# Kernel tuning notes

Measured on AMD Instinct MI355X. Metric: run time of the kernel, lower is better.

Reference implementation:

```python
import jax, jax.numpy as jnp
import numpy as np

N_NODES = 50000
N_EDGES = 800000
DIM_FEAT = 96
INFO_DIM = 32
DIM_EMB = 160
CONV_OUT = DIM_EMB - INFO_DIM  # 128
NUM_LAYERS = 3
NUM_GRAPHS = 500
DIM_TARGET = 10


def setup_inputs() -> dict:
    key = jax.random.key(0)
    ks = jax.random.split(key, 20)
    inp = {
        'x': jax.random.normal(ks[0], (N_NODES, DIM_FEAT), dtype=jnp.float32),
        'edge_index': jax.random.randint(ks[1], (2, N_EDGES), 0, N_NODES, dtype=jnp.int32),
        'batch': jnp.sort(jax.random.randint(ks[2], (N_NODES,), 0, NUM_GRAPHS, dtype=jnp.int32)),
        'struc_info': jax.random.normal(ks[3], (NUM_GRAPHS, INFO_DIM), dtype=jnp.float32),
    }
    # SAGEConv params per layer: lin_l (on aggregated neighbors, with bias), lin_r (on root, no bias)
    in_dims = [DIM_FEAT + INFO_DIM, DIM_EMB, DIM_EMB]
    k = 4
    for i, din in enumerate(in_dims):
        s = 1.0 / np.sqrt(din)
        inp[f'Wl{i}'] = jax.random.uniform(ks[k], (din, CONV_OUT), jnp.float32, -s, s); k += 1
        inp[f'Wr{i}'] = jax.random.uniform(ks[k], (din, CONV_OUT), jnp.float32, -s, s); k += 1
        inp[f'b{i}'] = jax.random.uniform(ks[k], (CONV_OUT,), jnp.float32, -s, s); k += 1
    s1 = 1.0 / np.sqrt(NUM_LAYERS * CONV_OUT)
    inp['Wfc1'] = jax.random.uniform(ks[k], (NUM_LAYERS * CONV_OUT, DIM_EMB), jnp.float32, -s1, s1); k += 1
    inp['bfc1'] = jax.random.uniform(ks[k], (DIM_EMB,), jnp.float32, -s1, s1); k += 1
    s2 = 1.0 / np.sqrt(DIM_EMB)
    inp['Wfc2'] = jax.random.uniform(ks[k], (DIM_EMB, DIM_TARGET), jnp.float32, -s2, s2); k += 1
    inp['bfc2'] = jax.random.uniform(ks[k], (DIM_TARGET,), jnp.float32, -s2, s2)
    return inp


def _sage_conv(h, src, dst, Wl, Wr, b, n_nodes):
    # PyG SAGEConv (mean aggr): out = lin_l(mean_{j in N(i)} x_j) + lin_r(x_i)
    agg = jax.ops.segment_sum(h[src], dst, num_segments=n_nodes)       # [N, D]
    deg = jax.ops.segment_sum(jnp.ones_like(dst, dtype=h.dtype), dst, num_segments=n_nodes)
    mean = agg / jnp.maximum(deg, 1.0)[:, None]
    return mean @ Wl + b + h @ Wr


def reference(x, edge_index, batch, struc_info, Wl0, Wr0, b0, Wl1, Wr1, b1, Wl2, Wr2, b2, Wfc1, bfc1, Wfc2, bfc2):
    n_nodes = x.shape[0]
    src, dst = edge_index[0], edge_index[1]
    info = struc_info[batch]                         # [N, info_dim] repeated per node
    params = [(Wl0, Wr0, b0), (Wl1, Wr1, b1), (Wl2, Wr2, b2)]
    h = x
    outs = []
    for (Wl, Wr, b) in params:
        h = _sage_conv(jnp.concatenate([h, info], axis=1), src, dst, Wl, Wr, b, n_nodes)
        outs.append(h)
    hcat = jnp.concatenate(outs, axis=1)             # [N, num_layers*conv_out]
    g = jax.ops.segment_max(hcat, batch, num_segments=struc_info.shape[0])  # global max pool
    z = jax.nn.relu(g @ Wfc1 + bfc1)
    return z @ Wfc2 + bfc2
```

## Files before the change

kernel.cpp:

```cpp
#include <hip/hip_runtime.h>
#include <hip/hip_bf16.h>
#include <float.h>

#define NN 50000
#define NE 800000
#define DF 96
#define DI 32
#define CO 128
#define NG 500
#define HC 384
#define F1I 384
#define F1O 160
#define F2O 10
#define CAPLOG 7

typedef unsigned int  u32;
typedef unsigned short u16;
typedef short bf16x8 __attribute__((ext_vector_type(8)));
typedef float f32x4  __attribute__((ext_vector_type(4)));

__device__ __forceinline__ u16 f2b(float f) {
    __hip_bfloat16 h = __float2bfloat16(f);
    return *reinterpret_cast<u16*>(&h);
}
__device__ __forceinline__ float b2f(u16 u) {
    return __uint_as_float(((u32)u) << 16);
}
__device__ __forceinline__ float blo(u32 u) { return __uint_as_float(u << 16); }
__device__ __forceinline__ float bhi(u32 u) { return __uint_as_float(u & 0xffff0000u); }

#define PB_EDGE   782
#define PB_STARTS 196
#define PB_CAST   4688
#define PB_WT0    96
#define PB_WT1    128
#define PB_WT2    128
#define PB_INFO   500
#define PREP_GRID (PB_EDGE + PB_STARTS + PB_CAST + PB_WT0 + PB_WT1 + PB_WT2 + 3 * PB_INFO)

__global__ __launch_bounds__(256) void k_prep(
        const float* __restrict__ x, const int* __restrict__ batch, const float* __restrict__ info,
        const int* __restrict__ src, const int* __restrict__ dst,
        const float* __restrict__ Wl0, const float* __restrict__ Wr0, const float* __restrict__ b0,
        const float* __restrict__ Wl1, const float* __restrict__ Wr1, const float* __restrict__ b1,
        const float* __restrict__ Wl2, const float* __restrict__ Wr2, const float* __restrict__ b2,
        int* __restrict__ cnt, u16* __restrict__ csr,
        int* __restrict__ start, u16* __restrict__ xb,
        u16* __restrict__ WT0, u16* __restrict__ WT1, u16* __restrict__ WT2,
        float* __restrict__ iQl0, float* __restrict__ iQr0,
        float* __restrict__ iQl1, float* __restrict__ iQr1,
        float* __restrict__ iQl2, float* __restrict__ iQr2) {
    int blk = blockIdx.x;
    int t = threadIdx.x;
    if (blk < PB_EDGE) {
        int base = (blk * 256 + t) * 4;
        if (base < NE) {
            int4 dv = *(const int4*)&dst[base];
            int4 sv = *(const int4*)&src[base];
            int p0 = atomicAdd(&cnt[dv.x], 1);
            int p1 = atomicAdd(&cnt[dv.y], 1);
            int p2 = atomicAdd(&cnt[dv.z], 1);
            int p3 = atomicAdd(&cnt[dv.w], 1);
            if (p0 < (1 << CAPLOG)) csr[(dv.x << CAPLOG) + p0] = (u16)sv.x;
            if (p1 < (1 << CAPLOG)) csr[(dv.y << CAPLOG) + p1] = (u16)sv.y;
            if (p2 < (1 << CAPLOG)) csr[(dv.z << CAPLOG) + p2] = (u16)sv.z;
            if (p3 < (1 << CAPLOG)) csr[(dv.w << CAPLOG) + p3] = (u16)sv.w;
        }
        return;
    }
    blk -= PB_EDGE;
    if (blk < PB_STARTS) {
        int i = blk * 256 + t;
        if (i >= NN) return;
        int b = batch[i];
        if (i == 0) { for (int g = 0; g <= b; ++g) start[g] = 0; }
        else {
            int p = batch[i - 1];
            if (p != b) for (int g = p + 1; g <= b; ++g) start[g] = i;
        }
        if (i == NN - 1) { for (int g = b + 1; g <= NG; ++g) start[g] = NN; }
        return;
    }
    blk -= PB_STARTS;
    if (blk < PB_CAST) {
        int tid = blk * 256 + t;
        if (tid >= NN * DF / 4) return;
        float4 v = *(const float4*)&x[tid * 4];
        ushort4 o;
        o.x = f2b(v.x); o.y = f2b(v.y); o.z = f2b(v.z); o.w = f2b(v.w);
        *(ushort4*)&xb[tid * 4] = o;
        return;
    }
    blk -= PB_CAST;
    if (blk < PB_WT0 + PB_WT1 + PB_WT2) {
        const float* Wl; const float* Wr; u16* WT; int K; int rel;
        if (blk < PB_WT0) { Wl = Wl0; Wr = Wr0; WT = WT0; K = 96;  rel = blk; }
        else if (blk < PB_WT0 + PB_WT1) { Wl = Wl1; Wr = Wr1; WT = WT1; K = 128; rel = blk - PB_WT0; }
        else { Wl = Wl2; Wr = Wr2; WT = WT2; K = 128; rel = blk - PB_WT0 - PB_WT1; }
        int tid = rel * 256 + t;
        if (tid >= 256 * K) return;
        int n = tid / K;
        int k = tid - n * K;
        float v = (n < CO) ? Wl[k * CO + n] : Wr[k * CO + (n - CO)];
        WT[tid] = f2b(v);
        return;
    }
    blk -= PB_WT0 + PB_WT1 + PB_WT2;
    {
        const float* Wl; const float* Wr; const float* bias; float* iQl; float* iQr; int Ktop; int g;
        if (blk < PB_INFO) { Wl = Wl0; Wr = Wr0; bias = b0; iQl = iQl0; iQr = iQr0; Ktop = 96;  g = blk; }
        else if (blk < 2 * PB_INFO) { Wl = Wl1; Wr = Wr1; bias = b1; iQl = iQl1; iQr = iQr1; Ktop = 128; g = blk - PB_INFO; }
        else { Wl = Wl2; Wr = Wr2; bias = b2; iQl = iQl2; iQr = iQr2; Ktop = 128; g = blk - 2 * PB_INFO; }
        int c = t & 127;
        int sel = t >> 7;
        const float* W = sel ? Wr : Wl;
        float a = sel ? bias[c] : 0.0f;
        for (int d = 0; d < DI; ++d)
            a += info[g * DI + d] * W[(Ktop + d) * CO + c];
        (sel ? iQr : iQl)[g * CO + c] = a;
    }
}

template<int K>
__global__ __launch_bounds__(256) void k_mfma(const u16* __restrict__ A,
                                              const u16* __restrict__ WTg,
                                              const int* __restrict__ batch,
                                              const float* __restrict__ iQl,
                                              const float* __restrict__ iQr,
                                              u16* __restrict__ zlp,
                                              u16* __restrict__ zq) {
    constexpr int PITCH = K + 8;
    __shared__ short lds[256 * PITCH];

    int tid  = threadIdx.x;
    int w    = tid >> 6;
    int lane = tid & 63;
    int quad = lane >> 4;
    int l15  = lane & 15;

    constexpr int CH = 256 * K / 8;
    const uint4* wp = (const uint4*)WTg;
    for (int c = tid; c < CH; c += 256) {
        int n  = c / (K / 8);
        int ko = (c - n * (K / 8)) * 8;
        *(uint4*)&lds[n * PITCH + ko] = wp[c];
    }
    __syncthreads();

    int i0 = blockIdx.x * 128 + w * 32;
    int r0 = i0 + l15;       if (r0 >= NN) r0 = NN - 1;
    int r1 = i0 + 16 + l15;  if (r1 >= NN) r1 = NN - 1;
    const short* A0 = (const short*)A + (size_t)r0 * K;
    const short* A1 = (const short*)A + (size_t)r1 * K;

    f32x4 acc[2][16];
#pragma unroll
    for (int rt = 0; rt < 2; ++rt)
#pragma unroll
        for (int ct = 0; ct < 16; ++ct)
            acc[rt][ct] = (f32x4){0.f, 0.f, 0.f, 0.f};

#pragma unroll
    for (int ks = 0; ks < K / 32; ++ks) {
        int ka = ks * 32 + quad * 8;
        bf16x8 a0 = *(const bf16x8*)(A0 + ka);
        bf16x8 a1 = *(const bf16x8*)(A1 + ka);
#pragma unroll
        for (int ct = 0; ct < 16; ++ct) {
            bf16x8 b = *(const bf16x8*)&lds[(ct * 16 + l15) * PITCH + ka];
            acc[0][ct] = __builtin_amdgcn_mfma_f32_16x16x32_bf16(a0, b, acc[0][ct], 0, 0, 0);
            acc[1][ct] = __builtin_amdgcn_mfma_f32_16x16x32_bf16(a1, b, acc[1][ct], 0, 0, 0);
        }
    }

#pragma unroll
    for (int rt = 0; rt < 2; ++rt) {
#pragma unroll
        for (int reg = 0; reg < 4; ++reg) {
            int row = i0 + rt * 16 + quad * 4 + reg;
            if (row < NN) {
                int b = batch[row];
                const float* ql = &iQl[b * CO];
                const float* qr = &iQr[b * CO];
                u16* lp = zlp + (size_t)row * CO;
                u16* qp = zq  + (size_t)row * CO;
#pragma unroll
                for (int ct = 0; ct < 8; ++ct) {
                    int col = ct * 16 + l15;
                    lp[col] = f2b(acc[rt][ct][reg] + ql[col]);
                }
#pragma unroll
                for (int ct = 8; ct < 16; ++ct) {
                    int col = ct * 16 + l15 - 128;
                    qp[col] = f2b(acc[rt][ct][reg] + qr[col]);
                }
            }
        }
    }
}

__device__ __forceinline__ void acc8(float* a, const uint4& u) {
    a[0] += blo(u.x); a[1] += bhi(u.x);
    a[2] += blo(u.y); a[3] += bhi(u.y);
    a[4] += blo(u.z); a[5] += bhi(u.z);
    a[6] += blo(u.w); a[7] += bhi(u.w);
}

__global__ __launch_bounds__(256) void k_gatherb(const u32* __restrict__ zlp, const u32* __restrict__ zq,
                                                 const int* __restrict__ cnt, const u16* __restrict__ csr,
                                                 u32* __restrict__ hout) {
    int wave = threadIdx.x >> 6;
    int lane = threadIdx.x & 63;
    int q    = lane >> 4;
    int l16  = lane & 15;
    int i = blockIdx.x * 4 + wave;
    if (i >= NN) return;
    int deg = cnt[i];
    int degc = min(deg, 1 << CAPLOG);
    int s0 = i << CAPLOG;
    int s1 = s0 + degc;

    const uint4* Z = (const uint4*)zlp;

    float a[8] = {0,0,0,0,0,0,0,0};
    float b[8] = {0,0,0,0,0,0,0,0};
    float c[8] = {0,0,0,0,0,0,0,0};
    float d[8] = {0,0,0,0,0,0,0,0};

    int e = s0;
    for (; e + 15 < s1; e += 16) {
        int n0 = csr[e + q];
        int n1 = csr[e + 4 + q];
        int n2 = csr[e + 8 + q];
        int n3 = csr[e + 12 + q];
        uint4 u0 = Z[(size_t)n0 * 16 + l16];
        uint4 u1 = Z[(size_t)n1 * 16 + l16];
        uint4 u2 = Z[(size_t)n2 * 16 + l16];
        uint4 u3 = Z[(size_t)n3 * 16 + l16];
        acc8(a, u0); acc8(b, u1); acc8(c, u2); acc8(d, u3);
    }
    for (; e < s1; e += 4) {
        if (e + q < s1) {
            int n0 = csr[e + q];
            uint4 u0 = Z[(size_t)n0 * 16 + l16];
            acc8(a, u0);
        }
    }
#pragma unroll
    for (int j = 0; j < 8; ++j) {
        a[j] += b[j] + c[j] + d[j];
        a[j] += __shfl_xor(a[j], 16);
        a[j] += __shfl_xor(a[j], 32);
    }
    if (q == 0) {
        float r = 1.0f / fmaxf((float)deg, 1.0f);
        uint4 qq = ((const uint4*)zq)[(size_t)i * 16 + l16];
        uint4 o;
        o.x = (u32)f2b(a[0] * r + blo(qq.x)) | ((u32)f2b(a[1] * r + bhi(qq.x)) << 16);
        o.y = (u32)f2b(a[2] * r + blo(qq.y)) | ((u32)f2b(a[3] * r + bhi(qq.y)) << 16);
        o.z = (u32)f2b(a[4] * r + blo(qq.z)) | ((u32)f2b(a[5] * r + bhi(qq.z)) << 16);
        o.w = (u32)f2b(a[6] * r + blo(qq.w)) | ((u32)f2b(a[7] * r + bhi(qq.w)) << 16);
        ((uint4*)hout)[(size_t)i * 16 + l16] = o;
    }
}

__global__ __launch_bounds__(384) void k_poolfc(const u32* __restrict__ h1, const u32* __restrict__ h2,
                                                const u32* __restrict__ h3, const int* __restrict__ start,
                                                const float* __restrict__ W1, const float* __restrict__ b1,
                                                const float* __restrict__ W2, const float* __restrict__ b2,
                                                float* __restrict__ out) {
    __shared__ float s_part[6][128];
    __shared__ float s_g[F1I];
    __shared__ float s_z[F1O];
    int gr = blockIdx.x;
    int t  = threadIdx.x;
    int w    = t >> 6;
    int lane = t & 63;
    int buf  = w % 3;
    int half = w / 3;
    const u32* hb = (buf == 0) ? h1 : (buf == 1) ? h2 : h3;
    int s = start[gr], e = start[gr + 1];
    int mid = (s + e) >> 1;
    int n0 = half ? mid : s;
    int n1 = half ? e : mid;

    float mlo[4], mhi[4];
#pragma unroll
    for (int j = 0; j < 4; ++j) { mlo[j] = -FLT_MAX; mhi[j] = -FLT_MAX; }
    int n = n0;
    for (; n + 3 < n1; n += 4) {
        u32 v0 = hb[(size_t)(n + 0) * 64 + lane];
        u32 v1 = hb[(size_t)(n + 1) * 64 + lane];
        u32 v2 = hb[(size_t)(n + 2) * 64 + lane];
        u32 v3 = hb[(size_t)(n + 3) * 64 + lane];
        mlo[0] = fmaxf(mlo[0], blo(v0)); mhi[0] = fmaxf(mhi[0], bhi(v0));
        mlo[1] = fmaxf(mlo[1], blo(v1)); mhi[1] = fmaxf(mhi[1], bhi(v1));
        mlo[2] = fmaxf(mlo[2], blo(v2)); mhi[2] = fmaxf(mhi[2], bhi(v2));
        mlo[3] = fmaxf(mlo[3], blo(v3)); mhi[3] = fmaxf(mhi[3], bhi(v3));
    }
    for (; n < n1; ++n) {
        u32 v0 = hb[(size_t)n * 64 + lane];
        mlo[0] = fmaxf(mlo[0], blo(v0)); mhi[0] = fmaxf(mhi[0], bhi(v0));
    }
    float lo = fmaxf(fmaxf(mlo[0], mlo[1]), fmaxf(mlo[2], mlo[3]));
    float hi = fmaxf(fmaxf(mhi[0], mhi[1]), fmaxf(mhi[2], mhi[3]));
    s_part[w][2 * lane]     = lo;
    s_part[w][2 * lane + 1] = hi;
    __syncthreads();
    {
        int buf2 = t >> 7, cc = t & 127;
        s_g[t] = fmaxf(s_part[buf2][cc], s_part[buf2 + 3][cc]);
    }
    __syncthreads();
    if (t < F1O) {
        float acc = b1[t];
        for (int k = 0; k < F1I; ++k) acc += s_g[k] * W1[k * F1O + t];
        s_z[t] = fmaxf(acc, 0.0f);
    }
    __syncthreads();
    if (t < F2O) {
        float a = b2[t];
        for (int k = 0; k < F1O; ++k) a += s_z[k] * W2[k * F2O + t];
        out[gr * F2O + t] = a;
    }
}

extern "C" void kernel_launch(void* const* d_in, const int* in_sizes, int n_in,
                              void* d_out, int out_size, void* d_ws, size_t ws_size,
                              hipStream_t stream) {
    const float* x     = (const float*)d_in[0];
    const int*   eidx  = (const int*)d_in[1];
    const int*   batch = (const int*)d_in[2];
    const float* info  = (const float*)d_in[3];
    const float* Wl0 = (const float*)d_in[4];
    const float* Wr0 = (const float*)d_in[5];
    const float* b0  = (const float*)d_in[6];
    const float* Wl1 = (const float*)d_in[7];
    const float* Wr1 = (const float*)d_in[8];
    const float* b1  = (const float*)d_in[9];
    const float* Wl2 = (const float*)d_in[10];
    const float* Wr2 = (const float*)d_in[11];
    const float* b2  = (const float*)d_in[12];
    const float* Wfc1  = (const float*)d_in[13];
    const float* bfc1  = (const float*)d_in[14];
    const float* Wfc2  = (const float*)d_in[15];
    const float* bfc2  = (const float*)d_in[16];
    float* out = (float*)d_out;

    const int* src = eidx;
    const int* dst = eidx + NE;

    char* W = (char*)d_ws;
    u16* xb     = (u16*)(W + 0);
    u16* h1     = (u16*)(W + 9600000);
    u16* h2     = (u16*)(W + 22400000);
    u16* h3     = (u16*)(W + 35200000);
    u16* zlp    = (u16*)(W + 48000000);
    u16* zq     = (u16*)(W + 60800000);
    u16* WT0    = (u16*)(W + 73600000);
    u16* WT1    = (u16*)(W + 73649152);
    u16* WT2    = (u16*)(W + 73714688);
    float* iQl0 = (float*)(W + 73780224);
    float* iQr0 = (float*)(W + 74036224);
    float* iQl1 = (float*)(W + 74292224);
    float* iQr1 = (float*)(W + 74548224);
    float* iQl2 = (float*)(W + 74804224);
    float* iQr2 = (float*)(W + 75060224);
    int* start  = (int*)(W + 75316224);
    int* cnt    = (int*)(W + 75318272);
    u16* csr    = (u16*)(W + 75518336);

    hipMemsetAsync(cnt, 0, NN * sizeof(int), stream);

    k_prep<<<PREP_GRID, 256, 0, stream>>>(x, batch, info, src, dst,
        Wl0, Wr0, b0, Wl1, Wr1, b1, Wl2, Wr2, b2,
        cnt, csr, start, xb, WT0, WT1, WT2, iQl0, iQr0, iQl1, iQr1, iQl2, iQr2);

    const int gGemm = (NN + 127) / 128;
    const int gGath = (NN + 3) / 4;

    k_mfma<96><<<gGemm, 256, 0, stream>>>(xb, WT0, batch, iQl0, iQr0, zlp, zq);
    k_gatherb<<<gGath, 256, 0, stream>>>((const u32*)zlp, (const u32*)zq, cnt, csr, (u32*)h1);

    k_mfma<128><<<gGemm, 256, 0, stream>>>(h1, WT1, batch, iQl1, iQr1, zlp, zq);
    k_gatherb<<<gGath, 256, 0, stream>>>((const u32*)zlp, (const u32*)zq, cnt, csr, (u32*)h2);

    k_mfma<128><<<gGemm, 256, 0, stream>>>(h2, WT2, batch, iQl2, iQr2, zlp, zq);
    k_gatherb<<<gGath, 256, 0, stream>>>((const u32*)zlp, (const u32*)zq, cnt, csr, (u32*)h3);

    k_poolfc<<<NG, 384, 0, stream>>>((const u32*)h1, (const u32*)h2, (const u32*)h3, start,
                                     Wfc1, bfc1, Wfc2, bfc2, out);
}
```

Baseline: 324.0 us.

## Build CSR via two-pass binning with LDS atomics instead of global atomics

Replaces the per-edge global atomic CSR fill with a two-stage bucket sort. Edges are first binned by destination range (256 nodes per bin) using shared-memory counters and one global atomic per bin per block. A new kernel then scatters each bin into the fixed-capacity CSR using LDS atomics and writes the counts. This removes heavy contention on global atomics, at the cost of an extra kernel launch and an intermediate buffer round trip.

New measurement: 300.5 us. 1.08x faster.

```diff
diff --git a/kernel.cpp b/kernel.cpp
--- a/kernel.cpp
+++ b/kernel.cpp
@@ -13,6 +13,9 @@
 #define F1O 160
 #define F2O 10
 #define CAPLOG 7
+#define NRANGE 196
+#define EPB 3125
+#define RCAPLOG 13
 
 typedef unsigned int  u32;
 typedef unsigned short u16;
@@ -29,14 +32,14 @@
 __device__ __forceinline__ float blo(u32 u) { return __uint_as_float(u << 16); }
 __device__ __forceinline__ float bhi(u32 u) { return __uint_as_float(u & 0xffff0000u); }
 
-#define PB_EDGE   782
+#define PB_BIN    256
 #define PB_STARTS 196
 #define PB_CAST   4688
 #define PB_WT0    96
 #define PB_WT1    128
 #define PB_WT2    128
 #define PB_INFO   500
-#define PREP_GRID (PB_EDGE + PB_STARTS + PB_CAST + PB_WT0 + PB_WT1 + PB_WT2 + 3 * PB_INFO)
+#define PREP_GRID (PB_BIN + PB_STARTS + PB_CAST + PB_WT0 + PB_WT1 + PB_WT2 + 3 * PB_INFO)
 
 __global__ __launch_bounds__(256) void k_prep(
         const float* __restrict__ x, const int* __restrict__ batch, const float* __restrict__ info,
@@ -44,31 +47,42 @@
         const float* __restrict__ Wl0, const float* __restrict__ Wr0, const float* __restrict__ b0,
         const float* __restrict__ Wl1, const float* __restrict__ Wr1, const float* __restrict__ b1,
         const float* __restrict__ Wl2, const float* __restrict__ Wr2, const float* __restrict__ b2,
-        int* __restrict__ cnt, u16* __restrict__ csr,
+        int* __restrict__ grescnt, u32* __restrict__ ebin,
         int* __restrict__ start, u16* __restrict__ xb,
         u16* __restrict__ WT0, u16* __restrict__ WT1, u16* __restrict__ WT2,
         float* __restrict__ iQl0, float* __restrict__ iQr0,
         float* __restrict__ iQl1, float* __restrict__ iQr1,
         float* __restrict__ iQl2, float* __restrict__ iQr2) {
+    __shared__ u32 pairs[EPB];
+    __shared__ int lcnt[256];
     int blk = blockIdx.x;
     int t = threadIdx.x;
-    if (blk < PB_EDGE) {
-        int base = (blk * 256 + t) * 4;
-        if (base < NE) {
-            int4 dv = *(const int4*)&dst[base];
-            int4 sv = *(const int4*)&src[base];
-            int p0 = atomicAdd(&cnt[dv.x], 1);
-            int p1 = atomicAdd(&cnt[dv.y], 1);
-            int p2 = atomicAdd(&cnt[dv.z], 1);
-            int p3 = atomicAdd(&cnt[dv.w], 1);
-            if (p0 < (1 << CAPLOG)) csr[(dv.x << CAPLOG) + p0] = (u16)sv.x;
-            if (p1 < (1 << CAPLOG)) csr[(dv.y << CAPLOG) + p1] = (u16)sv.y;
-            if (p2 < (1 << CAPLOG)) csr[(dv.z << CAPLOG) + p2] = (u16)sv.z;
-            if (p3 < (1 << CAPLOG)) csr[(dv.w << CAPLOG) + p3] = (u16)sv.w;
+    if (blk < PB_BIN) {
+        int base = blk * EPB;
+        lcnt[t] = 0;
+        __syncthreads();
+        for (int j = t; j < EPB; j += 256) {
+            int e = base + j;
+            int d = dst[e];
+            int s = src[e];
+            pairs[j] = ((u32)(d & 255) << 24) | ((u32)(d >> 8) << 16) | (u32)s;
+            atomicAdd(&lcnt[d >> 8], 1);
+        }
+        __syncthreads();
+        int myCnt = lcnt[t];
+        int myBase = atomicAdd(&grescnt[t * 16], myCnt);
+        __syncthreads();
+        lcnt[t] = myBase;
+        __syncthreads();
+        for (int j = t; j < EPB; j += 256) {
+            u32 p = pairs[j];
+            int r = (p >> 16) & 255;
+            int pos = atomicAdd(&lcnt[r], 1);
+            if (pos < (1 << RCAPLOG)) ebin[(r << RCAPLOG) + pos] = p;
         }
         return;
     }
-    blk -= PB_EDGE;
+    blk -= PB_BIN;
     if (blk < PB_STARTS) {
         int i = blk * 256 + t;
         if (i >= NN) return;
@@ -119,6 +133,28 @@
             a += info[g * DI + d] * W[(Ktop + d) * CO + c];
         (sel ? iQr : iQl)[g * CO + c] = a;
     }
+}
+
+__global__ __launch_bounds__(256) void k_binB(const u32* __restrict__ ebin,
+                                              const int* __restrict__ grescnt,
+                                              int* __restrict__ cnt, u16* __restrict__ csr) {
+    __shared__ int lcnt[256];
+    int r = blockIdx.x;
+    int t = threadIdx.x;
+    lcnt[t] = 0;
+    __syncthreads();
+    int total = grescnt[r * 16];
+    if (total > (1 << RCAPLOG)) total = 1 << RCAPLOG;
+    for (int j = t; j < total; j += 256) {
+        u32 p = ebin[(r << RCAPLOG) + j];
+        int dloc = p >> 24;
+        int rank = atomicAdd(&lcnt[dloc], 1);
+        int node = (r << 8) + dloc;
+        if (rank < (1 << CAPLOG)) csr[(node << CAPLOG) + rank] = (u16)(p & 0xffff);
+    }
+    __syncthreads();
+    int node = (r << 8) + t;
+    if (node < NN) cnt[node] = lcnt[t];
 }
 
 template<int K>
@@ -369,12 +405,16 @@
     int* start  = (int*)(W + 75316224);
     int* cnt    = (int*)(W + 75318272);
     u16* csr    = (u16*)(W + 75518336);
-
-    hipMemsetAsync(cnt, 0, NN * sizeof(int), stream);
+    u32* ebin   = (u32*)(W + 88318336);
+    int* grescnt= (int*)(W + 96706560);
+
+    hipMemsetAsync(grescnt, 0, 256 * 16 * sizeof(int), stream);
 
     k_prep<<<PREP_GRID, 256, 0, stream>>>(x, batch, info, src, dst,
         Wl0, Wr0, b0, Wl1, Wr1, b1, Wl2, Wr2, b2,
-        cnt, csr, start, xb, WT0, WT1, WT2, iQl0, iQr0, iQl1, iQr1, iQl2, iQr2);
+        grescnt, ebin, start, xb, WT0, WT1, WT2, iQl0, iQr0, iQl1, iQr1, iQl2, iQr2);
+
+    k_binB<<<NRANGE, 256, 0, stream>>>(ebin, grescnt, cnt, csr);
 
     const int gGemm = (NN + 127) / 128;
     const int gGath = (NN + 3) / 4;
```
